# Kernel tuning notes

Hardware: AMD Instinct MI355X
Metric: run time of the kernel (lower is better)

The kernel has to match this reference:

```python
import jax, jax.numpy as jnp
import numpy as np

SHAPE = (64, 64, 64)
N0 = 4000
K = 5  # subm conv kernel size -> 125 taps


def _neighbors(coors, shp):
    # coors: [N,4] int (b,z,y,x), batch=1. Returns [N,125] int32 neighbor row ids, -1 if absent.
    offs = np.stack(np.meshgrid(np.arange(-2, 3), np.arange(-2, 3), np.arange(-2, 3), indexing='ij'), -1).reshape(-1, 3)
    shp = np.asarray(shp)
    grid = -np.ones(tuple(shp), np.int32)
    grid[coors[:, 1], coors[:, 2], coors[:, 3]] = np.arange(len(coors), dtype=np.int32)
    nb = coors[:, None, 1:4] + offs[None]  # [N,125,3]
    valid = ((nb >= 0) & (nb < shp)).all(-1)
    nbc = np.clip(nb, 0, shp - 1)
    nbr = grid[nbc[..., 0], nbc[..., 1], nbc[..., 2]]
    return np.where(valid, nbr, -1).astype(np.int32)


def _pool_map(coors, shp):
    # kernel 2 stride 2 sparse max pool: parent cell = spatial // 2
    out_shp = [s // 2 for s in shp]
    sp = coors[:, 1:4] // 2
    lin = (sp[:, 0] * out_shp[1] + sp[:, 1]) * out_shp[2] + sp[:, 2]
    uniq, inv = np.unique(lin, return_inverse=True)
    z = uniq // (out_shp[1] * out_shp[2])
    r = uniq % (out_shp[1] * out_shp[2])
    nc = np.stack([np.zeros_like(z), z, r // out_shp[2], r % out_shp[2]], 1).astype(np.int32)
    return inv.astype(np.int32), nc, out_shp


_PAIRS = [(3, 64), (64, 64), (64, 96), (96, 96), (96, 128), (128, 128), (128, 160), (160, 160), (160, 192), (192, 192), (192, 224), (224, 224), (224, 256), (256, 256)]
_WNAMES = ['w0a', 'w0b', 'w1a', 'w1b', 'w2a', 'w2b', 'w3a', 'w3b', 'w4a', 'w4b', 'w5a', 'w5b', 'w6a', 'w6b']


def setup_inputs() -> dict:
    rng = np.random.RandomState(0)
    lin = rng.choice(SHAPE[0] * SHAPE[1] * SHAPE[2], N0, replace=False)
    z = lin // (SHAPE[1] * SHAPE[2])
    r = lin % (SHAPE[1] * SHAPE[2])
    coors = np.stack([np.zeros_like(z), z, r // SHAPE[2], r % SHAPE[2]], 1).astype(np.int32)
    inp = {}
    c, shp = coors, list(SHAPE)
    for l in range(7):
        inp['nbr%d' % l] = jnp.asarray(_neighbors(c, shp))
        if l < 6:
            pm, c, shp = _pool_map(c, shp)
            inp['pool%d' % l] = jnp.asarray(pm)
    key = jax.random.key(0)
    for name, (ci, co) in zip(_WNAMES, _PAIRS):
        key, k = jax.random.split(key)
        inp[name] = jax.random.normal(k, (K ** 3, ci, co), jnp.float32) * (K ** 3 * ci) ** -0.5
    key, kf = jax.random.split(key)
    inp['features'] = jax.random.normal(kf, (N0, 3), jnp.float32)
    inp['coors'] = jnp.asarray(coors)
    inp['batch_size'] = 1
    return inp


def _subm(feats, nbr, w):
    # gather-GEMM-scatter form of SubMConv3d (bias=False): out active set == in active set
    valid = nbr >= 0  # [N,125]
    g = jnp.take(feats, jnp.maximum(nbr, 0), axis=0)  # [N,125,Cin]
    g = jnp.where(valid[:, :, None], g, jnp.zeros((), feats.dtype))
    return jnp.einsum('nkc,kco->no', g, w)  # [N,Cout]


def reference(features, coors, batch_size, nbr0, nbr1, nbr2, nbr3, nbr4, nbr5, nbr6, pool0, pool1, pool2, pool3, pool4, pool5, w0a, w0b, w1a, w1b, w2a, w2b, w3a, w3b, w4a, w4b, w5a, w5b, w6a, w6b):
    nbrs = (nbr0, nbr1, nbr2, nbr3, nbr4, nbr5, nbr6)
    pools = (pool0, pool1, pool2, pool3, pool4, pool5)
    ws = ((w0a, w0b), (w1a, w1b), (w2a, w2b), (w3a, w3b), (w4a, w4b), (w5a, w5b), (w6a, w6b))
    x = features
    for l in range(7):
        x = _subm(x, nbrs[l], ws[l][0])
        x = _subm(x, nbrs[l], ws[l][1])
        if l < 6:
            # sparse max pool over active voxels of each 2x2x2 cell
            x = jax.ops.segment_max(x, pools[l], num_segments=nbrs[l + 1].shape[0])
    return x
```

## Files before the change

kernel.cpp:

```cpp
#include <hip/hip_runtime.h>
#include <stddef.h>
#include <stdint.h>

#define KTAPS 125

typedef _Float16 f16x8 __attribute__((ext_vector_type(8)));
typedef _Float16 f16x4 __attribute__((ext_vector_type(4)));
typedef float    f32x4 __attribute__((ext_vector_type(4)));

template<int NT>
__global__ __launch_bounds__(256) void subm_mfma(
    const _Float16* __restrict__ finh, const int* __restrict__ nbr,
    const _Float16* __restrict__ wt, _Float16* __restrict__ Pout,
    int N, int CinP, int TS, int CS, int SWZ)
{
    constexpr int BN = NT * 32;
    constexpr int DEPTH = (NT <= 5) ? 4 : 2;
    __shared__ int       nbs[16][64];
    __shared__ unsigned  msk[16][2];
    __shared__ unsigned char vtl[2][16];
    __shared__ int       vcs[2];
    __shared__ unsigned short sjc[2][128];

    const int tid  = threadIdx.x;
    const int lane = tid & 63;
    const int wid  = tid >> 6;
    const int wy   = wid & 1;
    const int wx   = wid >> 1;
    const int r15  = lane & 15;
    const int g4   = lane >> 4;

    int rowtile, ts, cs;
    if (SWZ) {
        int L   = blockIdx.x;
        int q   = L >> 3;
        int TSo = TS >> 3;
        ts      = (L & 7) + 8 * (q % TSo);
        rowtile = q / TSo;
        cs      = 0;
    } else {
        rowtile = blockIdx.x; ts = blockIdx.y; cs = blockIdx.z;
    }

    const int row0 = rowtile * 64;
    const int k0   = (ts * KTAPS) / TS;
    const int k1   = ((ts + 1) * KTAPS) / TS;
    const int KR   = k1 - k0;
    const int CC   = CinP >> 5;
    const int cc0  = (cs * CC) / CS;
    const int cc1  = ((cs + 1) * CC) / CS;
    const int NC   = cc1 - cc0;

    #pragma unroll
    for (int p = 0; p < 4; ++p) {
        int e = tid + p * 256;
        if (e < KR * 64) {
            int j = e >> 6, r = e & 63;
            int gr = row0 + r;
            nbs[j][r] = (gr < N) ? nbr[(size_t)gr * KTAPS + k0 + j] : -1;
        }
    }
    __syncthreads();
    for (int j = wid; j < KR; j += 4) {
        unsigned long long m = __ballot(nbs[j][lane] >= 0);
        if (lane == 0) { msk[j][0] = (unsigned)m; msk[j][1] = (unsigned)(m >> 32); }
    }
    __syncthreads();
    if (wid < 2) {
        int c = 0;
        for (int j = 0; j < KR; ++j)
            if (msk[j][wid]) { if (lane == 0) vtl[wid][c] = (unsigned char)j; ++c; }
        if (lane == 0) vcs[wid] = c;
        int TT = c * NC;
        for (int t = lane; t < TT; t += 64) {
            int j = vtl[wid][t / NC];
            int cc = cc0 + (t - (t / NC) * NC);
            sjc[wid][t] = (unsigned short)((j << 8) | cc);
        }
    }
    __syncthreads();
    const int T = vcs[wy] * NC;

    f32x4 acc[2][NT];
    #pragma unroll
    for (int mt = 0; mt < 2; ++mt)
        #pragma unroll
        for (int nf = 0; nf < NT; ++nf)
            acc[mt][nf] = (f32x4){0.f, 0.f, 0.f, 0.f};

    if (T > 0) {
        const size_t wchunk = (size_t)32 * BN;
        const int    boffh  = (g4 * BN + wx * (NT * 16) + r15) * 8;

        auto LOADA = [&](f16x8 (&a)[2], int j, int c) {
            unsigned mm = __builtin_amdgcn_readfirstlane(msk[j][wy]);
            if (mm & 0xFFFFu) {
                int src = nbs[j][wy * 32 + r15];
                if (src < 0) src = N;
                a[0] = *(const f16x8*)(finh + (size_t)src * CinP + c * 32 + g4 * 8);
            }
            if (mm >> 16) {
                int src = nbs[j][wy * 32 + 16 + r15];
                if (src < 0) src = N;
                a[1] = *(const f16x8*)(finh + (size_t)src * CinP + c * 32 + g4 * 8);
            }
        };
        auto LOADB = [&](f16x8 (&b)[NT], int j, int c) {
            const _Float16* base = wt + ((size_t)(k0 + j) * CC + c) * wchunk;
            #pragma unroll
            for (int nf = 0; nf < NT; ++nf)
                b[nf] = *(const f16x8*)&base[boffh + nf * 128];
        };
        auto LD = [&](f16x8 (&a)[2], f16x8 (&b)[NT], int t) {
            if (t < T) {
                int e = sjc[wy][t];
                int j = e >> 8, c = e & 255;
                LOADA(a, j, c); LOADB(b, j, c);
            }
        };
        auto CP = [&](f16x8 (&a)[2], f16x8 (&b)[NT], int t) {
            int j = sjc[wy][t] >> 8;
            unsigned mm = __builtin_amdgcn_readfirstlane(msk[j][wy]);
            if (mm & 0xFFFFu)
                #pragma unroll
                for (int nf = 0; nf < NT; ++nf)
                    acc[0][nf] = __builtin_amdgcn_mfma_f32_16x16x32_f16(a[0], b[nf], acc[0][nf], 0, 0, 0);
            if (mm >> 16)
                #pragma unroll
                for (int nf = 0; nf < NT; ++nf)
                    acc[1][nf] = __builtin_amdgcn_mfma_f32_16x16x32_f16(a[1], b[nf], acc[1][nf], 0, 0, 0);
        };

        if constexpr (DEPTH == 4) {
            f16x8 A0[2], B0[NT], A1[2], B1[NT], A2[2], B2[NT], A3[2], B3[NT];
            LD(A0, B0, 0); LD(A1, B1, 1); LD(A2, B2, 2); LD(A3, B3, 3);
            int t = 0;
            while (true) {
                CP(A0, B0, t); LD(A0, B0, t + 4); if (++t >= T) break;
                CP(A1, B1, t); LD(A1, B1, t + 4); if (++t >= T) break;
                CP(A2, B2, t); LD(A2, B2, t + 4); if (++t >= T) break;
                CP(A3, B3, t); LD(A3, B3, t + 4); if (++t >= T) break;
            }
        } else {
            f16x8 A0[2], B0[NT], A1[2], B1[NT];
            LD(A0, B0, 0); LD(A1, B1, 1);
            int t = 0;
            while (true) {
                CP(A0, B0, t); LD(A0, B0, t + 2); if (++t >= T) break;
                CP(A1, B1, t); LD(A1, B1, t + 2); if (++t >= T) break;
            }
        }
    }

    _Float16* base = Pout + (size_t)(ts * CS + cs) * ((size_t)N * BN);
    #pragma unroll
    for (int mt = 0; mt < 2; ++mt) {
        #pragma unroll
        for (int q = 0; q < 4; ++q) {
            int r = row0 + wy * 32 + mt * 16 + g4 * 4 + q;
            if (r < N) {
                #pragma unroll
                for (int nf = 0; nf < NT; ++nf)
                    base[(size_t)r * BN + wx * (NT * 16) + nf * 16 + r15] =
                        (_Float16)acc[mt][nf][q];
            }
        }
    }
}

__global__ __launch_bounds__(256) void reduce_a(
    const _Float16* __restrict__ P, _Float16* __restrict__ H,
    int N, int BN, int S, float scale)
{
    const int qi = threadIdx.x & 15;
    const int st = threadIdx.x >> 4;
    const int q  = blockIdx.x * 16 + qi;
    const size_t i4  = (size_t)q * 4;
    const size_t tot = (size_t)N * BN;
    f32x4 s = (f32x4){0.f, 0.f, 0.f, 0.f};
    if (i4 < tot) {
        for (int si = st; si < S; si += 16) {
            f16x4 p = *(const f16x4*)&P[(size_t)si * tot + i4];
            s[0] += (float)p[0]; s[1] += (float)p[1];
            s[2] += (float)p[2]; s[3] += (float)p[3];
        }
    }
    __shared__ f32x4 red[16][16];
    red[st][qi] = s;
    __syncthreads();
    #pragma unroll
    for (int off = 8; off > 0; off >>= 1) {
        if (st < off) red[st][qi] += red[st + off][qi];
        __syncthreads();
    }
    if (st == 0 && i4 < (size_t)(N + 1) * BN) {
        f32x4 r = red[0][qi];
        f16x4 h;
        h[0] = (_Float16)(r[0] * scale); h[1] = (_Float16)(r[1] * scale);
        h[2] = (_Float16)(r[2] * scale); h[3] = (_Float16)(r[3] * scale);
        *(f16x4*)&H[i4] = h;
    }
}

__device__ __forceinline__ unsigned enc_f32(float f) {
    unsigned u = __float_as_uint(f);
    return (u & 0x80000000u) ? ~u : (u | 0x80000000u);
}

__global__ __launch_bounds__(256) void reduce_b(
    const _Float16* __restrict__ P, const int* __restrict__ pm,
    unsigned* __restrict__ ENC, float* __restrict__ dout,
    int N, int BN, int S, float fscale, int isLast)
{
    const int qi = threadIdx.x & 15;
    const int st = threadIdx.x >> 4;
    const int q  = blockIdx.x * 16 + qi;
    const size_t i4  = (size_t)q * 4;
    const size_t tot = (size_t)N * BN;
    f32x4 s = (f32x4){0.f, 0.f, 0.f, 0.f};
    if (i4 < tot) {
        for (int si = st; si < S; si += 16) {
            f16x4 p = *(const f16x4*)&P[(size_t)si * tot + i4];
            s[0] += (float)p[0]; s[1] += (float)p[1];
            s[2] += (float)p[2]; s[3] += (float)p[3];
        }
    }
    __shared__ f32x4 red[16][16];
    red[st][qi] = s;
    __syncthreads();
    #pragma unroll
    for (int off = 8; off > 0; off >>= 1) {
        if (st < off) red[st][qi] += red[st + off][qi];
        __syncthreads();
    }
    if (st == 0 && i4 < tot) {
        f32x4 r = red[0][qi];
        if (isLast) {
            dout[i4 + 0] = r[0] * fscale; dout[i4 + 1] = r[1] * fscale;
            dout[i4 + 2] = r[2] * fscale; dout[i4 + 3] = r[3] * fscale;
        } else {
            int row = (int)(i4 / BN), c = (int)(i4 % BN);
            unsigned* e = &ENC[(size_t)pm[row] * BN + c];
            atomicMax(e + 0, enc_f32(r[0]));
            atomicMax(e + 1, enc_f32(r[1]));
            atomicMax(e + 2, enc_f32(r[2]));
            atomicMax(e + 3, enc_f32(r[3]));
        }
    }
}

__global__ __launch_bounds__(256) void pool_dec(
    unsigned* __restrict__ ENC, _Float16* __restrict__ H, int Nout, int C, float scale)
{
    int i = blockIdx.x * 256 + threadIdx.x;
    if (i < Nout * C) {
        unsigned u = ENC[i];
        float f = __uint_as_float((u & 0x80000000u) ? (u ^ 0x80000000u) : ~u);
        H[i] = (_Float16)(f * scale);
        ENC[i] = 0u;
    } else if (i < (Nout + 1) * C) {
        H[i] = (_Float16)0.f;
    }
}

__global__ __launch_bounds__(256) void tap_flags(
    const int* n0, const int* n1, const int* n2, const int* n3,
    const int* n4, const int* n5, const int* n6,
    int N0, int N1, int N2, int N3, int N4, int N5, int N6,
    unsigned* __restrict__ flags)
{
    int l = blockIdx.y, k = blockIdx.x;
    const int* nb; int N;
    switch (l) {
        case 0: nb = n0; N = N0; break;  case 1: nb = n1; N = N1; break;
        case 2: nb = n2; N = N2; break;  case 3: nb = n3; N = N3; break;
        case 4: nb = n4; N = N4; break;  case 5: nb = n5; N = N5; break;
        default: nb = n6; N = N6; break;
    }
    bool any = false;
    for (int r = threadIdx.x; r < N; r += 256) any |= (nb[(size_t)r * KTAPS + k] >= 0);
    bool a = __syncthreads_or(any);
    if (threadIdx.x == 0) flags[l * KTAPS + k] = a ? 1u : 0u;
}

__global__ __launch_bounds__(256) void cvt_weights(
    const float* __restrict__ wa, const float* __restrict__ wb,
    _Float16* __restrict__ ta, _Float16* __restrict__ tb,
    const unsigned* __restrict__ flags,
    int CinA, int CCa, int CoutA, int splitA,
    int CinB, int CCb, int CoutB)
{
    int k = blockIdx.x;
    if (!flags[k]) return;
    int by = blockIdx.y;
    const float* w; _Float16* t; int Cin, CC, Cout, cc, c0;
    if (by < splitA) { w = wa; t = ta; Cin = CinA; CC = CCa; Cout = CoutA;
                       cc = by / (CoutA / 32); c0 = (by % (CoutA / 32)) * 32; }
    else { by -= splitA; w = wb; t = tb; Cin = CinB; CC = CCb; Cout = CoutB;
           cc = by / (CoutB / 32); c0 = (by % (CoutB / 32)) * 32; }

    __shared__ float T[32][33];
    int tid = threadIdx.x;
    #pragma unroll
    for (int p = 0; p < 4; ++p) {
        int e = tid + p * 256;
        int r = e >> 5, cl = e & 31;
        int ci = cc * 32 + r;
        T[r][cl] = (ci < Cin) ? w[((size_t)k * Cin + ci) * Cout + c0 + cl] : 0.f;
    }
    __syncthreads();
    if (tid < 128) {
        int g = tid >> 5, co = tid & 31;
        f16x8 h;
        #pragma unroll
        for (int j = 0; j < 8; ++j) h[j] = (_Float16)T[g * 8 + j][co];
        *(f16x8*)&t[((size_t)k * CC + cc) * (32 * (size_t)Cout) + ((size_t)g * Cout + c0 + co) * 8] = h;
    }
}

__global__ __launch_bounds__(256) void init_all(
    const float* __restrict__ feat, _Float16* __restrict__ H,
    unsigned* __restrict__ ENC, int N0, int nE)
{
    int i = blockIdx.x * 256 + threadIdx.x;
    if (i < nE) ENC[i] = 0u;
    int nH = (N0 + 1) * 32;
    if (i < nH) {
        int r = i >> 5, cl = i & 31;
        H[i] = (r < N0 && cl < 3) ? (_Float16)feat[r * 3 + cl] : (_Float16)0.f;
    }
}

static inline int round8(int x) { int r = ((x + 4) / 8) * 8; if (r < 8) r = 8; if (r > 56) r = 56; return r; }

static void conv_dispatch(int NT, dim3 g, hipStream_t s, const _Float16* fin, const int* nbr,
                          const _Float16* wt, _Float16* P, int N, int CinP, int TS, int CS, int SWZ)
{
    switch (NT) {
        case 2: subm_mfma<2><<<g,256,0,s>>>(fin,nbr,wt,P,N,CinP,TS,CS,SWZ); break;
        case 3: subm_mfma<3><<<g,256,0,s>>>(fin,nbr,wt,P,N,CinP,TS,CS,SWZ); break;
        case 4: subm_mfma<4><<<g,256,0,s>>>(fin,nbr,wt,P,N,CinP,TS,CS,SWZ); break;
        case 5: subm_mfma<5><<<g,256,0,s>>>(fin,nbr,wt,P,N,CinP,TS,CS,SWZ); break;
        case 6: subm_mfma<6><<<g,256,0,s>>>(fin,nbr,wt,P,N,CinP,TS,CS,SWZ); break;
        case 7: subm_mfma<7><<<g,256,0,s>>>(fin,nbr,wt,P,N,CinP,TS,CS,SWZ); break;
        case 8: subm_mfma<8><<<g,256,0,s>>>(fin,nbr,wt,P,N,CinP,TS,CS,SWZ); break;
    }
}

extern "C" void kernel_launch(void* const* d_in, const int* in_sizes, int n_in,
                              void* d_out, int out_size, void* d_ws, size_t ws_size,
                              hipStream_t stream)
{
    const int* nbr[7]; const int* pm[6]; int Ns[7];
    {
        int idx = 0;
        for (int l = 0; l < 7; ++l) {
            nbr[l] = (const int*)d_in[idx];
            Ns[l]  = in_sizes[idx] / KTAPS;
            ++idx;
            if (l < 6) { pm[l] = (const int*)d_in[idx]; ++idx; }
        }
    }
    const float* w[14];
    for (int i = 0; i < 14; ++i) w[i] = (const float*)d_in[13 + i];
    const float* feat = (const float*)d_in[27];

    static const int CI[14]  = {3,64, 64,96, 96,128, 128,160, 160,192, 192,224, 224,256};
    static const int CO[14]  = {64,64, 96,96, 128,128, 160,160, 192,192, 224,224, 256,256};
    static const int KSH[14] = {0,3, 2,2, 1,1, 0,0, 0,1, 0,2, 2,3};
    const float finalScale = 1.0f / 131072.0f;
    int CinP[14];
    for (int i = 0; i < 14; ++i) CinP[i] = (CI[i] < 32) ? 32 : CI[i];

    int TSv[14], CSv[14], SWv[14];
    size_t maxP = 0, maxHa = 0, maxHb = 0, maxE = 0, maxWA = 0, maxWB = 0;
    for (int l = 0; l < 7; ++l) {
        int rt = (Ns[l] + 63) / 64;
        for (int q = 0; q < 2; ++q) {
            int i = 2 * l + q;
            if (rt > 1) { TSv[i] = round8(1024 / rt); CSv[i] = 1; SWv[i] = 1; }
            else        { TSv[i] = KTAPS; CSv[i] = CinP[i] / 32; SWv[i] = 0; }
            size_t p = (size_t)TSv[i] * CSv[i] * Ns[l] * CO[i];
            if (p > maxP) maxP = p;
        }
        size_t ha = (size_t)(Ns[l] + 1) * CinP[2*l];   if (ha > maxHa) maxHa = ha;
        size_t hb = (size_t)(Ns[l] + 1) * CinP[2*l+1]; if (hb > maxHb) maxHb = hb;
        if (l < 6) { size_t e = (size_t)Ns[l+1] * CO[2*l+1]; if (e > maxE) maxE = e; }
        size_t wa = (size_t)KTAPS * CinP[2*l] * CO[2*l];     if (wa > maxWA) maxWA = wa;
        size_t wb = (size_t)KTAPS * CinP[2*l+1] * CO[2*l+1]; if (wb > maxWB) maxWB = wb;
    }
    size_t off = 0;
    auto carve = [&](size_t bytes) -> void* {
        void* p = (char*)d_ws + off;
        off = (off + bytes + 255) & ~(size_t)255;
        return p;
    };
    _Float16*  P    = (_Float16*)carve(maxP * 2);
    _Float16*  Ha   = (_Float16*)carve(maxHa * 2);
    _Float16*  Hb   = (_Float16*)carve(maxHb * 2);
    unsigned*  ENC  = (unsigned*)carve(maxE * 4);
    _Float16*  wtA  = (_Float16*)carve(maxWA * 2);
    _Float16*  wtB  = (_Float16*)carve(maxWB * 2);
    unsigned*  flags= (unsigned*)carve(7 * KTAPS * 4);

    {
        int nMax = (int)maxE;
        int nH = (Ns[0] + 1) * 32;
        if (nH > nMax) nMax = nH;
        init_all<<<(nMax + 255) / 256, 256, 0, stream>>>(feat, Ha, ENC, Ns[0], (int)maxE);
    }
    tap_flags<<<dim3(KTAPS, 7), 256, 0, stream>>>(
        nbr[0], nbr[1], nbr[2], nbr[3], nbr[4], nbr[5], nbr[6],
        Ns[0], Ns[1], Ns[2], Ns[3], Ns[4], Ns[5], Ns[6], flags);

    for (int l = 0; l < 7; ++l) {
        int ia = 2 * l, ib = 2 * l + 1;
        int N = Ns[l];
        int rt = (N + 63) / 64;
        int splitA = (CinP[ia] / 32) * (CO[ia] / 32);
        int splitB = (CinP[ib] / 32) * (CO[ib] / 32);
        cvt_weights<<<dim3(KTAPS, splitA + splitB), 256, 0, stream>>>(
            w[ia], w[ib], wtA, wtB, flags + l * KTAPS,
            CI[ia], CinP[ia] / 32, CO[ia], splitA,
            CI[ib], CinP[ib] / 32, CO[ib]);

        {
            int TS = TSv[ia], CS = CSv[ia], BN = CO[ia];
            dim3 g = SWv[ia] ? dim3(rt * TS) : dim3(rt, TS, CS);
            conv_dispatch(BN / 32, g, stream, Ha, nbr[l], wtA, P, N, CinP[ia], TS, CS, SWv[ia]);
            int quads = ((N + 1) * BN) / 4;
            reduce_a<<<(quads + 15) / 16, 256, 0, stream>>>(P, Hb, N, BN, TS * CS,
                                                            (float)(1 << KSH[ib]));
        }
        {
            int TS = TSv[ib], CS = CSv[ib], BN = CO[ib];
            dim3 g = SWv[ib] ? dim3(rt * TS) : dim3(rt, TS, CS);
            conv_dispatch(BN / 32, g, stream, Hb, nbr[l], wtB, P, N, CinP[ib], TS, CS, SWv[ib]);
            int quads = (N * BN) / 4;
            reduce_b<<<(quads + 15) / 16, 256, 0, stream>>>(
                P, (l < 6) ? pm[l] : nullptr, ENC, (float*)d_out,
                N, BN, TS * CS, finalScale, (l == 6) ? 1 : 0);
        }
        if (l < 6) {
            int C = CO[ib], Nout = Ns[l + 1];
            int tot2 = (Nout + 1) * C;
            pool_dec<<<(tot2 + 255) / 256, 256, 0, stream>>>(ENC, Ha, Nout, C,
                                                             (float)(1 << KSH[2 * l + 2]));
        }
    }
}
```

Baseline: 438.6 us.

## Replace shared-memory tap compaction and software pipeline with register-resident neighbor masks

Neighbor ids and per-half-wave validity masks now live in registers via ballot, which removes the shared-memory staging, three block barriers and the compacted (tap, chunk) schedule. The main loop becomes a plain unrolled walk over a fixed 8-tap or 1-tap slice with inline loads and MFMAs, replacing the hand-built 2/4-deep register prefetch. The multi-rowtile tap split is fixed at 16 instead of being derived from the row-tile count. This lowers setup and sync overhead but relies on the compiler for latency hiding and can change occupancy and the amount of split-K partial-sum traffic.

```diff
diff --git a/kernel.cpp b/kernel.cpp
--- a/kernel.cpp
+++ b/kernel.cpp
@@ -8,20 +8,13 @@
 typedef _Float16 f16x4 __attribute__((ext_vector_type(4)));
 typedef float    f32x4 __attribute__((ext_vector_type(4)));
 
-template<int NT>
+template<int NT, int KRC>
 __global__ __launch_bounds__(256) void subm_mfma(
     const _Float16* __restrict__ finh, const int* __restrict__ nbr,
     const _Float16* __restrict__ wt, _Float16* __restrict__ Pout,
-    int N, int CinP, int TS, int CS, int SWZ)
+    int N, int CinP, int TS, int CS)
 {
     constexpr int BN = NT * 32;
-    constexpr int DEPTH = (NT <= 5) ? 4 : 2;
-    __shared__ int       nbs[16][64];
-    __shared__ unsigned  msk[16][2];
-    __shared__ unsigned char vtl[2][16];
-    __shared__ int       vcs[2];
-    __shared__ unsigned short sjc[2][128];
-
     const int tid  = threadIdx.x;
     const int lane = tid & 63;
     const int wid  = tid >> 6;
@@ -31,15 +24,13 @@
     const int g4   = lane >> 4;
 
     int rowtile, ts, cs;
-    if (SWZ) {
-        int L   = blockIdx.x;
-        int q   = L >> 3;
-        int TSo = TS >> 3;
-        ts      = (L & 7) + 8 * (q % TSo);
-        rowtile = q / TSo;
-        cs      = 0;
+    if (KRC == 8) {
+        int L = blockIdx.x, q = L >> 3;
+        ts = (L & 7) + 8 * (q & 1);
+        rowtile = q >> 1;
+        cs = 0;
     } else {
-        rowtile = blockIdx.x; ts = blockIdx.y; cs = blockIdx.z;
+        rowtile = 0; ts = blockIdx.y; cs = blockIdx.z;
     }
 
     const int row0 = rowtile * 64;
@@ -49,37 +40,23 @@
     const int CC   = CinP >> 5;
     const int cc0  = (cs * CC) / CS;
     const int cc1  = ((cs + 1) * CC) / CS;
-    const int NC   = cc1 - cc0;
-
-    #pragma unroll
-    for (int p = 0; p < 4; ++p) {
-        int e = tid + p * 256;
-        if (e < KR * 64) {
-            int j = e >> 6, r = e & 63;
-            int gr = row0 + r;
-            nbs[j][r] = (gr < N) ? nbr[(size_t)gr * KTAPS + k0 + j] : -1;
-        }
-    }
-    __syncthreads();
-    for (int j = wid; j < KR; j += 4) {
-        unsigned long long m = __ballot(nbs[j][lane] >= 0);
-        if (lane == 0) { msk[j][0] = (unsigned)m; msk[j][1] = (unsigned)(m >> 32); }
-    }
-    __syncthreads();
-    if (wid < 2) {
-        int c = 0;
-        for (int j = 0; j < KR; ++j)
-            if (msk[j][wid]) { if (lane == 0) vtl[wid][c] = (unsigned char)j; ++c; }
-        if (lane == 0) vcs[wid] = c;
-        int TT = c * NC;
-        for (int t = lane; t < TT; t += 64) {
-            int j = vtl[wid][t / NC];
-            int cc = cc0 + (t - (t / NC) * NC);
-            sjc[wid][t] = (unsigned short)((j << 8) | cc);
-        }
-    }
-    __syncthreads();
-    const int T = vcs[wy] * NC;
+
+    int nb0[KRC], nb1[KRC];
+    unsigned m0[KRC], m1[KRC];
+    #pragma unroll
+    for (int j = 0; j < KRC; ++j) {
+        int v0 = -1, v1 = -1;
+        if (j < KR) {
+            int r0 = row0 + wy * 32 + r15;
+            int r1 = r0 + 16;
+            if (r0 < N) v0 = nbr[(size_t)r0 * KTAPS + k0 + j];
+            if (r1 < N) v1 = nbr[(size_t)r1 * KTAPS + k0 + j];
+        }
+        nb0[j] = (v0 < 0) ? N : v0;
+        nb1[j] = (v1 < 0) ? N : v1;
+        m0[j] = (unsigned)(__ballot(v0 >= 0) & 0xFFFFull);
+        m1[j] = (unsigned)(__ballot(v1 >= 0) & 0xFFFFull);
+    }
 
     f32x4 acc[2][NT];
     #pragma unroll
@@ -88,66 +65,23 @@
         for (int nf = 0; nf < NT; ++nf)
             acc[mt][nf] = (f32x4){0.f, 0.f, 0.f, 0.f};
 
-    if (T > 0) {
-        const size_t wchunk = (size_t)32 * BN;
-        const int    boffh  = (g4 * BN + wx * (NT * 16) + r15) * 8;
-
-        auto LOADA = [&](f16x8 (&a)[2], int j, int c) {
-            unsigned mm = __builtin_amdgcn_readfirstlane(msk[j][wy]);
-            if (mm & 0xFFFFu) {
-                int src = nbs[j][wy * 32 + r15];
-                if (src < 0) src = N;
-                a[0] = *(const f16x8*)(finh + (size_t)src * CinP + c * 32 + g4 * 8);
-            }
-            if (mm >> 16) {
-                int src = nbs[j][wy * 32 + 16 + r15];
-                if (src < 0) src = N;
-                a[1] = *(const f16x8*)(finh + (size_t)src * CinP + c * 32 + g4 * 8);
-            }
-        };
-        auto LOADB = [&](f16x8 (&b)[NT], int j, int c) {
-            const _Float16* base = wt + ((size_t)(k0 + j) * CC + c) * wchunk;
+    const size_t wchunk = (size_t)32 * BN;
+    const int    boffh  = (g4 * BN + wx * (NT * 16) + r15) * 8;
+
+    for (int cc = cc0; cc < cc1; ++cc) {
+        #pragma unroll
+        for (int j = 0; j < KRC; ++j) {
+            unsigned mm0 = m0[j], mm1 = m1[j];
+            if (!(mm0 | mm1)) continue;
+            f16x8 a0 = {}, a1 = {};
+            if (mm0) a0 = *(const f16x8*)(finh + (size_t)nb0[j] * CinP + cc * 32 + g4 * 8);
+            if (mm1) a1 = *(const f16x8*)(finh + (size_t)nb1[j] * CinP + cc * 32 + g4 * 8);
+            const _Float16* base = wt + ((size_t)(k0 + j) * CC + cc) * wchunk + boffh;
             #pragma unroll
-            for (int nf = 0; nf < NT; ++nf)
-                b[nf] = *(const f16x8*)&base[boffh + nf * 128];
-        };
-        auto LD = [&](f16x8 (&a)[2], f16x8 (&b)[NT], int t) {
-            if (t < T) {
-                int e = sjc[wy][t];
-                int j = e >> 8, c = e & 255;
-                LOADA(a, j, c); LOADB(b, j, c);
-            }
-        };
-        auto CP = [&](f16x8 (&a)[2], f16x8 (&b)[NT], int t) {
-            int j = sjc[wy][t] >> 8;
-            unsigned mm = __builtin_amdgcn_readfirstlane(msk[j][wy]);
-            if (mm & 0xFFFFu)
-                #pragma unroll
-                for (int nf = 0; nf < NT; ++nf)
-                    acc[0][nf] = __builtin_amdgcn_mfma_f32_16x16x32_f16(a[0], b[nf], acc[0][nf], 0, 0, 0);
-            if (mm >> 16)
-                #pragma unroll
-                for (int nf = 0; nf < NT; ++nf)
-                    acc[1][nf] = __builtin_amdgcn_mfma_f32_16x16x32_f16(a[1], b[nf], acc[1][nf], 0, 0, 0);
-        };
-
-        if constexpr (DEPTH == 4) {
-            f16x8 A0[2], B0[NT], A1[2], B1[NT], A2[2], B2[NT], A3[2], B3[NT];
-            LD(A0, B0, 0); LD(A1, B1, 1); LD(A2, B2, 2); LD(A3, B3, 3);
-            int t = 0;
-            while (true) {
-                CP(A0, B0, t); LD(A0, B0, t + 4); if (++t >= T) break;
-                CP(A1, B1, t); LD(A1, B1, t + 4); if (++t >= T) break;
-                CP(A2, B2, t); LD(A2, B2, t + 4); if (++t >= T) break;
-                CP(A3, B3, t); LD(A3, B3, t + 4); if (++t >= T) break;
-            }
-        } else {
-            f16x8 A0[2], B0[NT], A1[2], B1[NT];
-            LD(A0, B0, 0); LD(A1, B1, 1);
-            int t = 0;
-            while (true) {
-                CP(A0, B0, t); LD(A0, B0, t + 2); if (++t >= T) break;
-                CP(A1, B1, t); LD(A1, B1, t + 2); if (++t >= T) break;
+            for (int nf = 0; nf < NT; ++nf) {
+                f16x8 b = *(const f16x8*)(base + (size_t)nf * 128);
+                if (mm0) acc[0][nf] = __builtin_amdgcn_mfma_f32_16x16x32_f16(a0, b, acc[0][nf], 0, 0, 0);
+                if (mm1) acc[1][nf] = __builtin_amdgcn_mfma_f32_16x16x32_f16(a1, b, acc[1][nf], 0, 0, 0);
             }
         }
     }
@@ -331,19 +265,30 @@
     }
 }
 
-static inline int round8(int x) { int r = ((x + 4) / 8) * 8; if (r < 8) r = 8; if (r > 56) r = 56; return r; }
-
-static void conv_dispatch(int NT, dim3 g, hipStream_t s, const _Float16* fin, const int* nbr,
-                          const _Float16* wt, _Float16* P, int N, int CinP, int TS, int CS, int SWZ)
-{
-    switch (NT) {
-        case 2: subm_mfma<2><<<g,256,0,s>>>(fin,nbr,wt,P,N,CinP,TS,CS,SWZ); break;
-        case 3: subm_mfma<3><<<g,256,0,s>>>(fin,nbr,wt,P,N,CinP,TS,CS,SWZ); break;
-        case 4: subm_mfma<4><<<g,256,0,s>>>(fin,nbr,wt,P,N,CinP,TS,CS,SWZ); break;
-        case 5: subm_mfma<5><<<g,256,0,s>>>(fin,nbr,wt,P,N,CinP,TS,CS,SWZ); break;
-        case 6: subm_mfma<6><<<g,256,0,s>>>(fin,nbr,wt,P,N,CinP,TS,CS,SWZ); break;
-        case 7: subm_mfma<7><<<g,256,0,s>>>(fin,nbr,wt,P,N,CinP,TS,CS,SWZ); break;
-        case 8: subm_mfma<8><<<g,256,0,s>>>(fin,nbr,wt,P,N,CinP,TS,CS,SWZ); break;
+static void conv_dispatch(int NT, int krc8, dim3 g, hipStream_t s, const _Float16* fin,
+                          const int* nbr, const _Float16* wt, _Float16* P,
+                          int N, int CinP, int TS, int CS)
+{
+    if (krc8) {
+        switch (NT) {
+            case 2: subm_mfma<2,8><<<g,256,0,s>>>(fin,nbr,wt,P,N,CinP,TS,CS); break;
+            case 3: subm_mfma<3,8><<<g,256,0,s>>>(fin,nbr,wt,P,N,CinP,TS,CS); break;
+            case 4: subm_mfma<4,8><<<g,256,0,s>>>(fin,nbr,wt,P,N,CinP,TS,CS); break;
+            case 5: subm_mfma<5,8><<<g,256,0,s>>>(fin,nbr,wt,P,N,CinP,TS,CS); break;
+            case 6: subm_mfma<6,8><<<g,256,0,s>>>(fin,nbr,wt,P,N,CinP,TS,CS); break;
+            case 7: subm_mfma<7,8><<<g,256,0,s>>>(fin,nbr,wt,P,N,CinP,TS,CS); break;
+            case 8: subm_mfma<8,8><<<g,256,0,s>>>(fin,nbr,wt,P,N,CinP,TS,CS); break;
+        }
+    } else {
+        switch (NT) {
+            case 2: subm_mfma<2,1><<<g,256,0,s>>>(fin,nbr,wt,P,N,CinP,TS,CS); break;
+            case 3: subm_mfma<3,1><<<g,256,0,s>>>(fin,nbr,wt,P,N,CinP,TS,CS); break;
+            case 4: subm_mfma<4,1><<<g,256,0,s>>>(fin,nbr,wt,P,N,CinP,TS,CS); break;
+            case 5: subm_mfma<5,1><<<g,256,0,s>>>(fin,nbr,wt,P,N,CinP,TS,CS); break;
+            case 6: subm_mfma<6,1><<<g,256,0,s>>>(fin,nbr,wt,P,N,CinP,TS,CS); break;
+            case 7: subm_mfma<7,1><<<g,256,0,s>>>(fin,nbr,wt,P,N,CinP,TS,CS); break;
+            case 8: subm_mfma<8,1><<<g,256,0,s>>>(fin,nbr,wt,P,N,CinP,TS,CS); break;
+        }
     }
 }
 
@@ -372,14 +317,14 @@
     int CinP[14];
     for (int i = 0; i < 14; ++i) CinP[i] = (CI[i] < 32) ? 32 : CI[i];
 
-    int TSv[14], CSv[14], SWv[14];
+    int TSv[14], CSv[14], K8v[14];
     size_t maxP = 0, maxHa = 0, maxHb = 0, maxE = 0, maxWA = 0, maxWB = 0;
     for (int l = 0; l < 7; ++l) {
         int rt = (Ns[l] + 63) / 64;
         for (int q = 0; q < 2; ++q) {
             int i = 2 * l + q;
-            if (rt > 1) { TSv[i] = round8(1024 / rt); CSv[i] = 1; SWv[i] = 1; }
-            else        { TSv[i] = KTAPS; CSv[i] = CinP[i] / 32; SWv[i] = 0; }
+            if (rt > 1) { TSv[i] = 16; CSv[i] = 1; K8v[i] = 1; }
+            else        { TSv[i] = KTAPS; CSv[i] = CinP[i] / 32; K8v[i] = 0; }
             size_t p = (size_t)TSv[i] * CSv[i] * Ns[l] * CO[i];
             if (p > maxP) maxP = p;
         }
@@ -426,16 +371,16 @@
 
         {
             int TS = TSv[ia], CS = CSv[ia], BN = CO[ia];
-            dim3 g = SWv[ia] ? dim3(rt * TS) : dim3(rt, TS, CS);
-            conv_dispatch(BN / 32, g, stream, Ha, nbr[l], wtA, P, N, CinP[ia], TS, CS, SWv[ia]);
+            dim3 g = K8v[ia] ? dim3(rt * TS) : dim3(1, TS, CS);
+            conv_dispatch(BN / 32, K8v[ia], g, stream, Ha, nbr[l], wtA, P, N, CinP[ia], TS, CS);
             int quads = ((N + 1) * BN) / 4;
             reduce_a<<<(quads + 15) / 16, 256, 0, stream>>>(P, Hb, N, BN, TS * CS,
                                                             (float)(1 << KSH[ib]));
         }
         {
             int TS = TSv[ib], CS = CSv[ib], BN = CO[ib];
-            dim3 g = SWv[ib] ? dim3(rt * TS) : dim3(rt, TS, CS);
-            conv_dispatch(BN / 32, g, stream, Hb, nbr[l], wtB, P, N, CinP[ib], TS, CS, SWv[ib]);
+            dim3 g = K8v[ib] ? dim3(rt * TS) : dim3(1, TS, CS);
+            conv_dispatch(BN / 32, K8v[ib], g, stream, Hb, nbr[l], wtB, P, N, CinP[ib], TS, CS);
             int quads = (N * BN) / 4;
             reduce_b<<<(quads + 15) / 16, 256, 0, stream>>>(
                 P, (l < 6) ? pm[l] : nullptr, ENC, (float*)d_out,
```

New measurement: 543.2 us. 1.24x slower.
